# Performance work log

Hardware: AMD Instinct MI355X
Metric: run time of the kernel (lower is better)

The kernel has to match this reference:

```python
import jax, jax.numpy as jnp
import numpy as np

B = 32          # batch
NR = 1000       # n_reports
NP = 2000       # n_paths (candidate codes per lookup matrix)
NC = 3000       # n_codes (valid path / code entries)
NSNIP = 20000   # n_snippets
RV = 20000      # report word vocab
CV = 50000      # code word vocab
QL = 50         # report length (words)
S = 100         # num_snippet per code
L = 60          # len_snippet (words per snippet)
E = 300         # word embedding dim
DD = 100        # dim_dense
K = 5           # k_max_pool
NEG = 1.0e12


def setup_inputs() -> dict:
    key = jax.random.key(0)
    ks = jax.random.split(key, 16)
    f = jnp.float32
    sc = lambda n: 1.0 / float(np.sqrt(n))
    inp = {}
    inp["r_idx"] = jax.random.randint(ks[0], (B,), 0, NR)
    inp["c_idx"] = jax.random.randint(ks[1], (B,), 0, NP)
    # lookup tables stored as float (cast to int inside forward, as in torch)
    inp["matrix"] = jax.random.randint(ks[2], (NR, NP), 0, NC).astype(f)
    inp["report_table"] = jax.random.randint(ks[3], (NR, QL), 0, RV).astype(f)
    inp["report_word_emb"] = jax.random.normal(ks[4], (RV, E), dtype=f)
    inp["idf_table"] = jax.random.uniform(ks[5], (RV, 1), dtype=f, minval=0.5, maxval=6.0)
    inp["code_table"] = jax.random.randint(ks[6], (NC, S), 0, NSNIP).astype(f)
    inp["snippet_table"] = jax.random.randint(ks[7], (NSNIP, L), 0, CV).astype(f)
    inp["code_word_emb"] = jax.random.normal(ks[8], (CV, E), dtype=f)
    inp["snippet_len_table"] = jax.random.randint(ks[9], (NSNIP, 1), 1, L + 1).astype(f)
    inp["code_len_table"] = jax.random.randint(ks[10], (NP, 1), 1, S + 1).astype(f)
    # trainable relevance MLP + k-max fusion
    inp["W1"] = jax.random.uniform(ks[11], (E, DD), dtype=f, minval=-sc(E), maxval=sc(E))
    inp["b1"] = jnp.zeros((DD,), f)
    inp["W2"] = jax.random.uniform(ks[12], (DD, DD // 2), dtype=f, minval=-sc(DD), maxval=sc(DD))
    inp["b2"] = jnp.zeros((DD // 2,), f)
    inp["W3"] = jax.random.uniform(ks[13], (DD // 2, 1), dtype=f, minval=-sc(DD // 2), maxval=sc(DD // 2))
    inp["b3"] = jnp.zeros((1,), f)
    inp["Wk"] = jax.random.uniform(ks[14], (K, 1), dtype=f, minval=-sc(K), maxval=sc(K))
    inp["bk"] = jnp.zeros((1,), f)
    return inp


def _l2norm(x, axis):
    n = jnp.linalg.norm(x, ord=2, axis=axis, keepdims=True)
    y = x / n
    return jnp.where(jnp.isnan(y), 0.0, y)  # torch: NaN-fix after div


def reference(r_idx, c_idx, matrix, report_table, report_word_emb, idf_table,
              code_table, snippet_table, code_word_emb, snippet_len_table,
              code_len_table, W1, b1, W2, b2, W3, b3, Wk, bk):
    trans_c = matrix[r_idx, c_idx].astype(jnp.int32)            # (b,)
    r_vec = report_table[r_idx].astype(jnp.int32)               # (b,q)
    r_emb = report_word_emb[r_vec]                              # (b,q,e)
    c_snip = code_table[trans_c].astype(jnp.int32)              # (b,s)
    s_len = snippet_len_table[c_snip, 0].astype(jnp.int32)      # (b,s)
    c_words = snippet_table[c_snip].astype(jnp.int32)           # (b,s,l)
    c_emb = code_word_emb[c_words]                              # (b,s,l,e)
    s_mask = jnp.arange(L)[None, None, :] < s_len[:, :, None]   # (b,s,l)
    # masked dot attention: every report word attends within each snippet
    scores = jnp.einsum('bqe,bsle->bqsl', r_emb, c_emb)
    scores = scores - (~s_mask)[:, None, :, :].astype(scores.dtype) * NEG
    a = jax.nn.softmax(scores, axis=3)
    attn_v = jnp.einsum('bqsl,bsle->bqse', a, c_emb)            # (b,q,s,e)
    nc = _l2norm(attn_v, 3)                                     # (b,q,s,e)
    nr = _l2norm(r_emb, 2)                                      # (b,q,e)
    rc = nr[:, :, None, :] * nc                                 # (b,q,s,e)
    h = jnp.tanh(rc @ W1 + b1)
    h = jnp.tanh(h @ W2 + b2)
    rel = jnp.tanh(h @ W3 + b3)[..., 0]                         # (b,q,s)
    c_len = code_len_table[c_idx, 0].astype(jnp.int32)          # (b,)
    c_mask = (jnp.arange(S)[None, :] < c_len[:, None]).astype(rel.dtype)
    rel = rel * c_mask[:, None, :]
    topk = jax.lax.top_k(rel, K)[0]                             # (b,q,k)
    r_c = (topk @ Wk + bk)[..., 0]                              # (b,q)
    r_idf = idf_table[r_vec, 0]                                 # (b,q)
    r_idf = jnp.where(r_idf == 0.0, -NEG, r_idf)
    r_idf = jax.nn.softmax(r_idf, axis=1)
    return jnp.sum(r_c * r_idf, axis=1)                         # (b,)
```

## Files before the change

### kernel.cpp

```cpp
#include <hip/hip_runtime.h>
#include <math.h>

typedef __attribute__((ext_vector_type(8))) _Float16 half8;
typedef __attribute__((ext_vector_type(4))) _Float16 half4v;
typedef __attribute__((ext_vector_type(4))) float f32x4;

constexpr int cB = 32, cNP = 2000, cS = 100, cL = 60, cE = 300;
constexpr int cQ = 50, cDD = 100, cDH = 50;
constexpr float cNEG = 1.0e12f;

constexpr size_t OFF_REL  = 0;
constexpr size_t OFF_RG   = 160000;
constexpr size_t OFF_RNRM = 640000;
constexpr size_t OFF_IDFW = 641600;
constexpr size_t OFF_W1TH = 643200;
constexpr size_t OFF_W1TL = 660224;
constexpr size_t OFF_W2TH = 677248;
constexpr size_t OFF_W2TL = 681344;

constexpr int LDS_CL    = 0;
constexpr int LDS_AL    = 72000;
constexpr int LDS_AVF   = 84000;
constexpr int LDS_G_HI  = 0;
constexpr int LDS_G_LO  = 40960;
constexpr int LDS_H1    = 84000;
constexpr int LDS_H2    = 116768;
constexpr int LDS_SCL   = 144000;
constexpr int LDS_WORDS = 144256;
constexpr int LDS_TOTAL = 144512;

__device__ __forceinline__ _Float16 h_hi(float f) { return (_Float16)f; }
__device__ __forceinline__ _Float16 h_lo(float f, _Float16 h) { return (_Float16)(f - (float)h); }
__device__ __forceinline__ int bswz(int cb, int row) {
    return (cb & ~127) | ((cb & 127) ^ ((row & 7) << 4));
}

__global__ void prep_weights(const float* __restrict__ W1, const float* __restrict__ W2,
                             _Float16* __restrict__ W1TH, _Float16* __restrict__ W1TL,
                             _Float16* __restrict__ W2TH, _Float16* __restrict__ W2TL)
{
    int tid = blockIdx.x * blockDim.x + threadIdx.x;
    int stride = gridDim.x * blockDim.x;
    for (int idx = tid; idx < 112 * 304; idx += stride) {
        int d = idx / 304, e = idx % 304;
        float w = (d < cDD && e < cE) ? W1[(size_t)e * cDD + d] : 0.f;
        _Float16 h = h_hi(w);
        W1TH[idx] = h; W1TL[idx] = h_lo(w, h);
    }
    for (int idx = tid; idx < 64 * 128; idx += stride) {
        int j = idx / 128, d = idx % 128;
        float w = (j < cDH && d < cDD) ? W2[(size_t)d * cDH + j] : 0.f;
        _Float16 h = h_hi(w);
        W2TH[idx] = h; W2TL[idx] = h_lo(w, h);
    }
}

__global__ __launch_bounds__(256) void prep_batch(
    const int* __restrict__ r_idx,
    const float* __restrict__ report_table,
    const float* __restrict__ report_word_emb,
    const float* __restrict__ idf_table,
    float* __restrict__ Rg, float* __restrict__ rnorm, float* __restrict__ idfw)
{
    int b = blockIdx.x, tid = threadIdx.x;
    __shared__ int rv[cQ];
    if (tid < cQ) rv[tid] = (int)report_table[(size_t)r_idx[b] * cQ + tid];
    __syncthreads();
    float* dst = Rg + (size_t)b * cQ * cE;
    for (int idx = tid; idx < cQ * 75; idx += 256) {
        int q = idx / 75, e4 = idx % 75;
        f32x4 v = *(const f32x4*)(report_word_emb + (size_t)rv[q] * cE + e4 * 4);
        *(f32x4*)(dst + (size_t)q * cE + e4 * 4) = v;
    }
    __syncthreads();
    if (tid < cQ) {
        const float* row = dst + (size_t)tid * cE;
        float ss = 0.f;
        for (int e = 0; e < cE; e += 4) {
            f32x4 v = *(const f32x4*)(row + e);
            ss += v[0]*v[0] + v[1]*v[1] + v[2]*v[2] + v[3]*v[3];
        }
        rnorm[b * cQ + tid] = sqrtf(ss);
    }
    if (tid < 64) {
        float x = -INFINITY;
        if (tid < cQ) {
            float w = idf_table[rv[tid]];
            x = (w == 0.0f) ? -cNEG : w;
        }
        float m = x;
        for (int o = 32; o; o >>= 1) m = fmaxf(m, __shfl_xor(m, o));
        float e = (tid < cQ) ? expf(x - m) : 0.f;
        float ssum = e;
        for (int o = 32; o; o >>= 1) ssum += __shfl_xor(ssum, o);
        if (tid < cQ) idfw[b * cQ + tid] = e / ssum;
    }
}

__global__ __launch_bounds__(512, 1) void kernelA(
    const int* __restrict__ r_idx, const int* __restrict__ c_idx,
    const float* __restrict__ matrix, const float* __restrict__ code_table,
    const float* __restrict__ snippet_table, const float* __restrict__ code_word_emb,
    const float* __restrict__ snippet_len_table,
    const float* __restrict__ Rg, const float* __restrict__ rnorm,
    const _Float16* __restrict__ W1TH, const _Float16* __restrict__ W1TL, const float* __restrict__ b1,
    const _Float16* __restrict__ W2TH, const _Float16* __restrict__ W2TL, const float* __restrict__ b2,
    const float* __restrict__ W3, const float* __restrict__ b3,
    float* __restrict__ rel_out)
{
    const int s = blockIdx.x, b = blockIdx.y;
    const int tid = threadIdx.x;
    const int lane = tid & 63, wid = tid >> 6;
    const int n = lane & 15, gl = lane >> 4;

    __shared__ __align__(16) unsigned char smem[LDS_TOTAL];
    int*   words = (int*)(smem + LDS_WORDS);
    float* sclp  = (float*)(smem + LDS_SCL);
    float* Cl    = (float*)(smem + LDS_CL);
    float* Alp   = (float*)(smem + LDS_AL);
    float* AVf   = (float*)(smem + LDS_AVF);

    const int rr = r_idx[b], cc = c_idx[b];
    const int code = (int)matrix[(size_t)rr * cNP + cc];
    const int snip = (int)code_table[(size_t)code * cS + s];
    const int slen = (int)snippet_len_table[snip];

    if (tid < cL) words[tid] = (int)snippet_table[(size_t)snip * cL + tid];
    if (tid < cQ) sclp[tid] = 0.f;
    __syncthreads();

    for (int idx = tid; idx < cL * 75; idx += 512) {
        int l = idx / 75, e4 = idx % 75;
        f32x4 v = *(const f32x4*)(code_word_emb + (size_t)words[l] * cE + e4 * 4);
        *(f32x4*)(Cl + l * 300 + e4 * 4) = v;
    }
    __syncthreads();

    {
        const int qt = tid >> 5, lt2 = tid & 31;
        float acc[4][2];
        #pragma unroll
        for (int i = 0; i < 4; i++)
            #pragma unroll
            for (int j = 0; j < 2; j++) acc[i][j] = 0.f;
        const float* rbase = Rg + (size_t)b * cQ * cE;
        const float* rrow[4];
        #pragma unroll
        for (int i = 0; i < 4; i++) {
            int q = qt + 16 * i;
            rrow[i] = rbase + (size_t)(q < cQ ? q : 0) * cE;
        }
        int lrow[2];
        #pragma unroll
        for (int j = 0; j < 2; j++) {
            int l = lt2 + 32 * j;
            lrow[j] = (l < cL) ? l : 0;
        }
        for (int e = 0; e < cE; e += 4) {
            f32x4 rv[4], cv[2];
            #pragma unroll
            for (int i = 0; i < 4; i++) rv[i] = *(const f32x4*)(rrow[i] + e);
            #pragma unroll
            for (int j = 0; j < 2; j++) cv[j] = *(const f32x4*)(Cl + lrow[j] * 300 + e);
            #pragma unroll
            for (int i = 0; i < 4; i++)
                #pragma unroll
                for (int j = 0; j < 2; j++)
                    acc[i][j] += rv[i][0] * cv[j][0] + rv[i][1] * cv[j][1] +
                                 rv[i][2] * cv[j][2] + rv[i][3] * cv[j][3];
        }
        #pragma unroll
        for (int i = 0; i < 4; i++) {
            int q = qt + 16 * i;
            if (q >= cQ) continue;
            #pragma unroll
            for (int j = 0; j < 2; j++) {
                int l = lt2 + 32 * j;
                if (l >= cL) continue;
                Alp[q * 60 + l] = acc[i][j] - ((l >= slen) ? cNEG : 0.f);
            }
        }
    }
    __syncthreads();

    {
        const int g2 = tid >> 2, k = tid & 3;
        if (g2 < cQ) {
            float v[15];
            float m = -INFINITY;
            #pragma unroll
            for (int t = 0; t < 15; t++) { v[t] = Alp[g2 * 60 + k + 4 * t]; m = fmaxf(m, v[t]); }
            m = fmaxf(m, __shfl_xor(m, 1));
            m = fmaxf(m, __shfl_xor(m, 2));
            float sum = 0.f;
            #pragma unroll
            for (int t = 0; t < 15; t++) { v[t] = expf(v[t] - m); sum += v[t]; }
            sum += __shfl_xor(sum, 1);
            sum += __shfl_xor(sum, 2);
            float inv = 1.0f / sum;
            #pragma unroll
            for (int t = 0; t < 15; t++) Alp[g2 * 60 + k + 4 * t] = v[t] * inv;
        }
    }
    __syncthreads();

    {
        const int qt3 = tid >> 5, et3 = tid & 31;
        const float* arow[4];
        int qv[4];
        #pragma unroll
        for (int i = 0; i < 4; i++) {
            int q = qt3 + 16 * i;
            qv[i] = q;
            arow[i] = Alp + (size_t)((q < cQ) ? q : 0) * 60;
        }
        int e4v[3], e4c[3];
        #pragma unroll
        for (int jj = 0; jj < 3; jj++) {
            e4v[jj] = et3 + 32 * jj;
            e4c[jj] = (e4v[jj] < 75) ? e4v[jj] : 0;
        }
        f32x4 acc4[4][3];
        #pragma unroll
        for (int i = 0; i < 4; i++)
            #pragma unroll
            for (int jj = 0; jj < 3; jj++) acc4[i][jj] = (f32x4){0.f, 0.f, 0.f, 0.f};
        for (int l = 0; l < cL; l++) {
            float av[4];
            #pragma unroll
            for (int i = 0; i < 4; i++) av[i] = arow[i][l];
            f32x4 cv[3];
            #pragma unroll
            for (int jj = 0; jj < 3; jj++) cv[jj] = *(const f32x4*)(Cl + l * 300 + e4c[jj] * 4);
            #pragma unroll
            for (int i = 0; i < 4; i++)
                #pragma unroll
                for (int jj = 0; jj < 3; jj++) {
                    acc4[i][jj][0] += av[i] * cv[jj][0];
                    acc4[i][jj][1] += av[i] * cv[jj][1];
                    acc4[i][jj][2] += av[i] * cv[jj][2];
                    acc4[i][jj][3] += av[i] * cv[jj][3];
                }
        }
        #pragma unroll
        for (int i = 0; i < 4; i++)
            #pragma unroll
            for (int jj = 0; jj < 3; jj++)
                if (e4v[jj] < 75 && qv[i] < cQ)
                    *(f32x4*)(AVf + qv[i] * 300 + e4v[jj] * 4) = acc4[i][jj];
    }
    __syncthreads();

    if (tid < 256) {
        const int qs = tid >> 4, es = tid & 15;
        #pragma unroll
        for (int jj = 0; jj < 5; jj++) {
            int e4 = es + 16 * jj;
            int e4cl = (e4 < 75) ? e4 : 0;
            #pragma unroll
            for (int i = 0; i < 4; i++) {
                int q = qs + 16 * i;
                int qcl = (q < cQ) ? q : 0;
                f32x4 v = *(const f32x4*)(AVf + qcl * 300 + e4cl * 4);
                bool valid = (e4 < 75) && (q < cQ);
                float dv = valid ? (v[0]*v[0] + v[1]*v[1] + v[2]*v[2] + v[3]*v[3]) : 0.f;
                dv += __shfl_xor(dv, 1);
                dv += __shfl_xor(dv, 2);
                dv += __shfl_xor(dv, 4);
                dv += __shfl_xor(dv, 8);
                if (es == 0 && q < cQ) sclp[q] += dv;
            }
        }
    }
    __syncthreads();

    if (tid < cQ) {
        float p = rnorm[b * cQ + tid] * sqrtf(sclp[tid]);
        sclp[tid] = (p > 0.f) ? (1.0f / p) : 0.f;
    }

    {
        const float* RgB = Rg + (size_t)b * cQ * cE;
        for (int idx = tid; idx < 64 * 80; idx += 512) {
            int q = idx / 80, e4 = idx % 80;
            half4v h4 = {0, 0, 0, 0}, l4 = {0, 0, 0, 0};
            if (q < cQ && e4 < 75) {
                f32x4 av4 = *(const f32x4*)(AVf + q * 300 + e4 * 4);
                f32x4 rv4 = *(const f32x4*)(RgB + (size_t)q * cE + e4 * 4);
                #pragma unroll
                for (int k = 0; k < 4; k++) {
                    float gf = av4[k] * rv4[k];
                    h4[k] = h_hi(gf);
                    l4[k] = h_lo(gf, h4[k]);
                }
            }
            int bo = q * 640 + bswz(8 * e4, q);
            *(half4v*)(smem + LDS_G_HI + bo) = h4;
            *(half4v*)(smem + LDS_G_LO + bo) = l4;
        }
    }
    __syncthreads();

    {
        const half8 z8 = {0,0,0,0,0,0,0,0};
        const int dt = wid;
        f32x4 accH[4];
        #pragma unroll
        for (int q2 = 0; q2 < 4; q2++) accH[q2] = (f32x4){0.f, 0.f, 0.f, 0.f};
        if (dt < 7) {
            #pragma unroll
            for (int ks = 0; ks < 10; ks++) {
                bool lv = (ks != 9) || (gl < 2);
                half8 gh[4], glo[4];
                #pragma unroll
                for (int q2 = 0; q2 < 4; q2++) {
                    gh[q2] = z8; glo[q2] = z8;
                    if (lv) {
                        int q = 16 * q2 + n;
                        int bo = q * 640 + bswz(64 * ks + 16 * gl, q);
                        gh[q2]  = *(const half8*)(smem + LDS_G_HI + bo);
                        glo[q2] = *(const half8*)(smem + LDS_G_LO + bo);
                    }
                }
                half8 wh = z8, wl = z8;
                if (lv) {
                    int d = 16 * dt + n;
                    wh = *(const half8*)(W1TH + (size_t)d * 304 + 32 * ks + 8 * gl);
                    wl = *(const half8*)(W1TL + (size_t)d * 304 + 32 * ks + 8 * gl);
                }
                #pragma unroll
                for (int q2 = 0; q2 < 4; q2++) {
                    accH[q2] = __builtin_amdgcn_mfma_f32_16x16x32_f16(gh[q2],  wh, accH[q2], 0, 0, 0);
                    accH[q2] = __builtin_amdgcn_mfma_f32_16x16x32_f16(gh[q2],  wl, accH[q2], 0, 0, 0);
                    accH[q2] = __builtin_amdgcn_mfma_f32_16x16x32_f16(glo[q2], wh, accH[q2], 0, 0, 0);
                }
            }
        }
        float* h1p = (float*)(smem + LDS_H1);
        if (dt < 7) {
            int d = 16 * dt + n;
            #pragma unroll
            for (int q2 = 0; q2 < 4; q2++)
                #pragma unroll
                for (int r = 0; r < 4; r++) {
                    int q = 16 * q2 + 4 * gl + r;
                    if (q < cQ) {
                        float v = (d < cDD) ? tanhf(accH[q2][r] * sclp[q] + b1[d]) : 0.f;
                        h1p[q * 128 + d] = v;
                    }
                }
        }
        for (int idx = tid; idx < cQ * 16; idx += 512) {
            int q = idx >> 4, d = 112 + (idx & 15);
            h1p[q * 128 + d] = 0.f;
        }
    }
    __syncthreads();

    {
        const float* h1p = (const float*)(smem + LDS_H1);
        const int jw = 16 * (wid & 3) + n;
        const int q2b = (wid >> 2) * 2;
        f32x4 accJ[2];
        #pragma unroll
        for (int t = 0; t < 2; t++) accJ[t] = (f32x4){0.f, 0.f, 0.f, 0.f};
        #pragma unroll
        for (int ks = 0; ks < 4; ks++) {
            half8 hh[2], hl[2];
            #pragma unroll
            for (int t = 0; t < 2; t++) {
                int q = 16 * (q2b + t) + n;
                const float* p = h1p + q * 128 + 32 * ks + 8 * gl;
                f32x4 fa = *(const f32x4*)p;
                f32x4 fb = *(const f32x4*)(p + 4);
                half8 h8, l8;
                #pragma unroll
                for (int jj = 0; jj < 8; jj++) {
                    float f = (jj < 4) ? fa[jj] : fb[jj - 4];
                    _Float16 h = h_hi(f);
                    h8[jj] = h;
                    l8[jj] = h_lo(f, h);
                }
                hh[t] = h8; hl[t] = l8;
            }
            half8 wh = *(const half8*)(W2TH + (size_t)jw * 128 + 32 * ks + 8 * gl);
            half8 wl = *(const half8*)(W2TL + (size_t)jw * 128 + 32 * ks + 8 * gl);
            #pragma unroll
            for (int t = 0; t < 2; t++) {
                accJ[t] = __builtin_amdgcn_mfma_f32_16x16x32_f16(hh[t], wh, accJ[t], 0, 0, 0);
                accJ[t] = __builtin_amdgcn_mfma_f32_16x16x32_f16(hh[t], wl, accJ[t], 0, 0, 0);
                accJ[t] = __builtin_amdgcn_mfma_f32_16x16x32_f16(hl[t], wh, accJ[t], 0, 0, 0);
            }
        }
        float* h2p = (float*)(smem + LDS_H2);
        #pragma unroll
        for (int t = 0; t < 2; t++)
            #pragma unroll
            for (int r = 0; r < 4; r++) {
                int q = 16 * (q2b + t) + 4 * gl + r;
                if (q < cQ && jw < cDH) h2p[q * 68 + jw] = tanhf(accJ[t][r] + b2[jw]);
            }
    }
    __syncthreads();

    if (tid < cQ) {
        const float* h2p = (const float*)(smem + LDS_H2);
        float a = b3[0];
        #pragma unroll 10
        for (int jj = 0; jj < cDH; jj++) a += h2p[tid * 68 + jj] * W3[jj];
        rel_out[((size_t)b * cQ + tid) * cS + s] = tanhf(a);
    }
}

__global__ __launch_bounds__(64) void kernelB(
    const float* __restrict__ rel_ws, const float* __restrict__ idfw,
    const int* __restrict__ c_idx, const float* __restrict__ code_len_table,
    const float* __restrict__ Wk, const float* __restrict__ bk,
    float* __restrict__ out)
{
    int b = blockIdx.x, q = threadIdx.x;
    float val = 0.f;
    if (q < cQ) {
        int clen = (int)code_len_table[c_idx[b]];
        const float* row = rel_ws + ((size_t)b * cQ + q) * cS;
        float t0 = -INFINITY, t1 = -INFINITY, t2 = -INFINITY, t3 = -INFINITY, t4 = -INFINITY;
        for (int s = 0; s < cS; s++) {
            float v = row[s] * ((s < clen) ? 1.f : 0.f);
            float m0 = fmaxf(t0, v), n0 = fminf(t0, v);
            float m1 = fmaxf(t1, n0), n1 = fminf(t1, n0);
            float m2 = fmaxf(t2, n1), n2 = fminf(t2, n1);
            float m3 = fmaxf(t3, n2), n3 = fminf(t3, n2);
            float m4 = fmaxf(t4, n3);
            t0 = m0; t1 = m1; t2 = m2; t3 = m3; t4 = m4;
        }
        float rc = t0 * Wk[0] + t1 * Wk[1] + t2 * Wk[2] + t3 * Wk[3] + t4 * Wk[4] + bk[0];
        val = rc * idfw[b * cQ + q];
    }
    for (int o = 32; o; o >>= 1) val += __shfl_down(val, o);
    if (q == 0) out[b] = val;
}

extern "C" void kernel_launch(void* const* d_in, const int* in_sizes, int n_in,
                              void* d_out, int out_size, void* d_ws, size_t ws_size,
                              hipStream_t stream)
{
    const int*   r_idx             = (const int*)d_in[0];
    const int*   c_idx             = (const int*)d_in[1];
    const float* matrix            = (const float*)d_in[2];
    const float* report_table      = (const float*)d_in[3];
    const float* report_word_emb   = (const float*)d_in[4];
    const float* idf_table         = (const float*)d_in[5];
    const float* code_table        = (const float*)d_in[6];
    const float* snippet_table     = (const float*)d_in[7];
    const float* code_word_emb     = (const float*)d_in[8];
    const float* snippet_len_table = (const float*)d_in[9];
    const float* code_len_table    = (const float*)d_in[10];
    const float* W1 = (const float*)d_in[11];
    const float* b1 = (const float*)d_in[12];
    const float* W2 = (const float*)d_in[13];
    const float* b2 = (const float*)d_in[14];
    const float* W3 = (const float*)d_in[15];
    const float* b3 = (const float*)d_in[16];
    const float* Wk = (const float*)d_in[17];
    const float* bk = (const float*)d_in[18];
    float* out = (float*)d_out;
    float* ws  = (float*)d_ws;

    float* rel_ws = ws + OFF_REL;
    float* Rg     = ws + OFF_RG;
    float* rnormp = ws + OFF_RNRM;
    float* idfwp  = ws + OFF_IDFW;
    _Float16* W1THp = (_Float16*)(ws + OFF_W1TH);
    _Float16* W1TLp = (_Float16*)(ws + OFF_W1TL);
    _Float16* W2THp = (_Float16*)(ws + OFF_W2TH);
    _Float16* W2TLp = (_Float16*)(ws + OFF_W2TL);

    prep_weights<<<64, 256, 0, stream>>>(W1, W2, W1THp, W1TLp, W2THp, W2TLp);
    prep_batch<<<cB, 256, 0, stream>>>(r_idx, report_table, report_word_emb, idf_table,
                                       Rg, rnormp, idfwp);
    kernelA<<<dim3(cS, cB), 512, 0, stream>>>(r_idx, c_idx, matrix, code_table,
                                              snippet_table, code_word_emb, snippet_len_table,
                                              Rg, rnormp,
                                              W1THp, W1TLp, b1, W2THp, W2TLp, b2, W3, b3, rel_ws);
    kernelB<<<cB, 64, 0, stream>>>(rel_ws, idfwp, c_idx, code_len_table, Wk, bk, out);
}
```

Measured before the change: 622.1 us.

## Double kernelA block to 1024 threads and stage report embeddings in LDS

Launches kernelA with 1024 threads per block instead of 512. Every stage's per-thread work is halved: fewer query rows per thread in the score and attention GEMMs, and fewer MFMA tiles per wave in the MLP layers. The report embedding rows are now copied into LDS, reusing the AVf region before it is written, so the score loop reads LDS instead of global memory. The aim is more waves in flight to hide latency. The trade-off is a tighter register budget under the new launch bounds, and a larger block can limit how many blocks fit on a CU.

New measurement: 558.0 us. -10.3%, faster.

```diff
diff --git a/kernel.cpp b/kernel.cpp
--- a/kernel.cpp
+++ b/kernel.cpp
@@ -97,7 +97,7 @@
     }
 }
 
-__global__ __launch_bounds__(512, 1) void kernelA(
+__global__ __launch_bounds__(1024, 4) void kernelA(
     const int* __restrict__ r_idx, const int* __restrict__ c_idx,
     const float* __restrict__ matrix, const float* __restrict__ code_table,
     const float* __restrict__ snippet_table, const float* __restrict__ code_word_emb,
@@ -119,6 +119,7 @@
     float* Cl    = (float*)(smem + LDS_CL);
     float* Alp   = (float*)(smem + LDS_AL);
     float* AVf   = (float*)(smem + LDS_AVF);
+    float* Rlds  = (float*)(smem + LDS_AVF);
 
     const int rr = r_idx[b], cc = c_idx[b];
     const int code = (int)matrix[(size_t)rr * cNP + cc];
@@ -127,9 +128,16 @@
 
     if (tid < cL) words[tid] = (int)snippet_table[(size_t)snip * cL + tid];
     if (tid < cQ) sclp[tid] = 0.f;
-    __syncthreads();
-
-    for (int idx = tid; idx < cL * 75; idx += 512) {
+    {
+        const float* RgB = Rg + (size_t)b * cQ * cE;
+        for (int idx = tid; idx < cQ * 75; idx += 1024) {
+            int q = idx / 75, e4 = idx % 75;
+            *(f32x4*)(Rlds + q * 300 + e4 * 4) = *(const f32x4*)(RgB + (size_t)q * cE + e4 * 4);
+        }
+    }
+    __syncthreads();
+
+    for (int idx = tid; idx < cL * 75; idx += 1024) {
         int l = idx / 75, e4 = idx % 75;
         f32x4 v = *(const f32x4*)(code_word_emb + (size_t)words[l] * cE + e4 * 4);
         *(f32x4*)(Cl + l * 300 + e4 * 4) = v;
@@ -138,17 +146,16 @@
 
     {
         const int qt = tid >> 5, lt2 = tid & 31;
-        float acc[4][2];
-        #pragma unroll
-        for (int i = 0; i < 4; i++)
+        float acc[2][2];
+        #pragma unroll
+        for (int i = 0; i < 2; i++)
             #pragma unroll
             for (int j = 0; j < 2; j++) acc[i][j] = 0.f;
-        const float* rbase = Rg + (size_t)b * cQ * cE;
-        const float* rrow[4];
-        #pragma unroll
-        for (int i = 0; i < 4; i++) {
-            int q = qt + 16 * i;
-            rrow[i] = rbase + (size_t)(q < cQ ? q : 0) * cE;
+        const float* rrow[2];
+        #pragma unroll
+        for (int i = 0; i < 2; i++) {
+            int q = qt + 32 * i;
+            rrow[i] = Rlds + (size_t)(q < cQ ? q : 0) * 300;
         }
         int lrow[2];
         #pragma unroll
@@ -157,21 +164,21 @@
             lrow[j] = (l < cL) ? l : 0;
         }
         for (int e = 0; e < cE; e += 4) {
-            f32x4 rv[4], cv[2];
-            #pragma unroll
-            for (int i = 0; i < 4; i++) rv[i] = *(const f32x4*)(rrow[i] + e);
+            f32x4 rv[2], cv[2];
+            #pragma unroll
+            for (int i = 0; i < 2; i++) rv[i] = *(const f32x4*)(rrow[i] + e);
             #pragma unroll
             for (int j = 0; j < 2; j++) cv[j] = *(const f32x4*)(Cl + lrow[j] * 300 + e);
             #pragma unroll
-            for (int i = 0; i < 4; i++)
+            for (int i = 0; i < 2; i++)
                 #pragma unroll
                 for (int j = 0; j < 2; j++)
                     acc[i][j] += rv[i][0] * cv[j][0] + rv[i][1] * cv[j][1] +
                                  rv[i][2] * cv[j][2] + rv[i][3] * cv[j][3];
         }
         #pragma unroll
-        for (int i = 0; i < 4; i++) {
-            int q = qt + 16 * i;
+        for (int i = 0; i < 2; i++) {
+            int q = qt + 32 * i;
             if (q >= cQ) continue;
             #pragma unroll
             for (int j = 0; j < 2; j++) {
@@ -206,11 +213,11 @@
 
     {
         const int qt3 = tid >> 5, et3 = tid & 31;
-        const float* arow[4];
-        int qv[4];
-        #pragma unroll
-        for (int i = 0; i < 4; i++) {
-            int q = qt3 + 16 * i;
+        const float* arow[2];
+        int qv[2];
+        #pragma unroll
+        for (int i = 0; i < 2; i++) {
+            int q = qt3 + 32 * i;
             qv[i] = q;
             arow[i] = Alp + (size_t)((q < cQ) ? q : 0) * 60;
         }
@@ -220,20 +227,20 @@
             e4v[jj] = et3 + 32 * jj;
             e4c[jj] = (e4v[jj] < 75) ? e4v[jj] : 0;
         }
-        f32x4 acc4[4][3];
-        #pragma unroll
-        for (int i = 0; i < 4; i++)
+        f32x4 acc4[2][3];
+        #pragma unroll
+        for (int i = 0; i < 2; i++)
             #pragma unroll
             for (int jj = 0; jj < 3; jj++) acc4[i][jj] = (f32x4){0.f, 0.f, 0.f, 0.f};
         for (int l = 0; l < cL; l++) {
-            float av[4];
-            #pragma unroll
-            for (int i = 0; i < 4; i++) av[i] = arow[i][l];
+            float av[2];
+            #pragma unroll
+            for (int i = 0; i < 2; i++) av[i] = arow[i][l];
             f32x4 cv[3];
             #pragma unroll
             for (int jj = 0; jj < 3; jj++) cv[jj] = *(const f32x4*)(Cl + l * 300 + e4c[jj] * 4);
             #pragma unroll
-            for (int i = 0; i < 4; i++)
+            for (int i = 0; i < 2; i++)
                 #pragma unroll
                 for (int jj = 0; jj < 3; jj++) {
                     acc4[i][jj][0] += av[i] * cv[jj][0];
@@ -243,7 +250,7 @@
                 }
         }
         #pragma unroll
-        for (int i = 0; i < 4; i++)
+        for (int i = 0; i < 2; i++)
             #pragma unroll
             for (int jj = 0; jj < 3; jj++)
                 if (e4v[jj] < 75 && qv[i] < cQ)
@@ -281,7 +288,7 @@
 
     {
         const float* RgB = Rg + (size_t)b * cQ * cE;
-        for (int idx = tid; idx < 64 * 80; idx += 512) {
+        for (int idx = tid; idx < 64 * 80; idx += 1024) {
             int q = idx / 80, e4 = idx % 80;
             half4v h4 = {0, 0, 0, 0}, l4 = {0, 0, 0, 0};
             if (q < cQ && e4 < 75) {
@@ -303,23 +310,24 @@
 
     {
         const half8 z8 = {0,0,0,0,0,0,0,0};
-        const int dt = wid;
-        f32x4 accH[4];
-        #pragma unroll
-        for (int q2 = 0; q2 < 4; q2++) accH[q2] = (f32x4){0.f, 0.f, 0.f, 0.f};
+        const int dt = wid & 7;
+        const int q2b = (wid >> 3) * 2;
+        f32x4 accH[2];
+        #pragma unroll
+        for (int t = 0; t < 2; t++) accH[t] = (f32x4){0.f, 0.f, 0.f, 0.f};
         if (dt < 7) {
             #pragma unroll
             for (int ks = 0; ks < 10; ks++) {
                 bool lv = (ks != 9) || (gl < 2);
-                half8 gh[4], glo[4];
-                #pragma unroll
-                for (int q2 = 0; q2 < 4; q2++) {
-                    gh[q2] = z8; glo[q2] = z8;
+                half8 gh[2], glo[2];
+                #pragma unroll
+                for (int t = 0; t < 2; t++) {
+                    gh[t] = z8; glo[t] = z8;
                     if (lv) {
-                        int q = 16 * q2 + n;
+                        int q = 16 * (q2b + t) + n;
                         int bo = q * 640 + bswz(64 * ks + 16 * gl, q);
-                        gh[q2]  = *(const half8*)(smem + LDS_G_HI + bo);
-                        glo[q2] = *(const half8*)(smem + LDS_G_LO + bo);
+                        gh[t]  = *(const half8*)(smem + LDS_G_HI + bo);
+                        glo[t] = *(const half8*)(smem + LDS_G_LO + bo);
                     }
                 }
                 half8 wh = z8, wl = z8;
@@ -329,10 +337,10 @@
                     wl = *(const half8*)(W1TL + (size_t)d * 304 + 32 * ks + 8 * gl);
                 }
                 #pragma unroll
-                for (int q2 = 0; q2 < 4; q2++) {
-                    accH[q2] = __builtin_amdgcn_mfma_f32_16x16x32_f16(gh[q2],  wh, accH[q2], 0, 0, 0);
-                    accH[q2] = __builtin_amdgcn_mfma_f32_16x16x32_f16(gh[q2],  wl, accH[q2], 0, 0, 0);
-                    accH[q2] = __builtin_amdgcn_mfma_f32_16x16x32_f16(glo[q2], wh, accH[q2], 0, 0, 0);
+                for (int t = 0; t < 2; t++) {
+                    accH[t] = __builtin_amdgcn_mfma_f32_16x16x32_f16(gh[t],  wh, accH[t], 0, 0, 0);
+                    accH[t] = __builtin_amdgcn_mfma_f32_16x16x32_f16(gh[t],  wl, accH[t], 0, 0, 0);
+                    accH[t] = __builtin_amdgcn_mfma_f32_16x16x32_f16(glo[t], wh, accH[t], 0, 0, 0);
                 }
             }
         }
@@ -340,17 +348,17 @@
         if (dt < 7) {
             int d = 16 * dt + n;
             #pragma unroll
-            for (int q2 = 0; q2 < 4; q2++)
+            for (int t = 0; t < 2; t++)
                 #pragma unroll
                 for (int r = 0; r < 4; r++) {
-                    int q = 16 * q2 + 4 * gl + r;
+                    int q = 16 * (q2b + t) + 4 * gl + r;
                     if (q < cQ) {
-                        float v = (d < cDD) ? tanhf(accH[q2][r] * sclp[q] + b1[d]) : 0.f;
+                        float v = (d < cDD) ? tanhf(accH[t][r] * sclp[q] + b1[d]) : 0.f;
                         h1p[q * 128 + d] = v;
                     }
                 }
         }
-        for (int idx = tid; idx < cQ * 16; idx += 512) {
+        for (int idx = tid; idx < cQ * 16; idx += 1024) {
             int q = idx >> 4, d = 112 + (idx & 15);
             h1p[q * 128 + d] = 0.f;
         }
@@ -360,46 +368,34 @@
     {
         const float* h1p = (const float*)(smem + LDS_H1);
         const int jw = 16 * (wid & 3) + n;
-        const int q2b = (wid >> 2) * 2;
-        f32x4 accJ[2];
-        #pragma unroll
-        for (int t = 0; t < 2; t++) accJ[t] = (f32x4){0.f, 0.f, 0.f, 0.f};
+        const int q2 = wid >> 2;
+        f32x4 accJ = (f32x4){0.f, 0.f, 0.f, 0.f};
         #pragma unroll
         for (int ks = 0; ks < 4; ks++) {
-            half8 hh[2], hl[2];
-            #pragma unroll
-            for (int t = 0; t < 2; t++) {
-                int q = 16 * (q2b + t) + n;
-                const float* p = h1p + q * 128 + 32 * ks + 8 * gl;
-                f32x4 fa = *(const f32x4*)p;
-                f32x4 fb = *(const f32x4*)(p + 4);
-                half8 h8, l8;
-                #pragma unroll
-                for (int jj = 0; jj < 8; jj++) {
-                    float f = (jj < 4) ? fa[jj] : fb[jj - 4];
-                    _Float16 h = h_hi(f);
-                    h8[jj] = h;
-                    l8[jj] = h_lo(f, h);
-                }
-                hh[t] = h8; hl[t] = l8;
+            int q = 16 * q2 + n;
+            const float* p = h1p + q * 128 + 32 * ks + 8 * gl;
+            f32x4 fa = *(const f32x4*)p;
+            f32x4 fb = *(const f32x4*)(p + 4);
+            half8 h8, l8;
+            #pragma unroll
+            for (int jj = 0; jj < 8; jj++) {
+                float f = (jj < 4) ? fa[jj] : fb[jj - 4];
+                _Float16 h = h_hi(f);
+                h8[jj] = h;
+                l8[jj] = h_lo(f, h);
             }
             half8 wh = *(const half8*)(W2TH + (size_t)jw * 128 + 32 * ks + 8 * gl);
             half8 wl = *(const half8*)(W2TL + (size_t)jw * 128 + 32 * ks + 8 * gl);
-            #pragma unroll
-            for (int t = 0; t < 2; t++) {
-                accJ[t] = __builtin_amdgcn_mfma_f32_16x16x32_f16(hh[t], wh, accJ[t], 0, 0, 0);
-                accJ[t] = __builtin_amdgcn_mfma_f32_16x16x32_f16(hh[t], wl, accJ[t], 0, 0, 0);
-                accJ[t] = __builtin_amdgcn_mfma_f32_16x16x32_f16(hl[t], wh, accJ[t], 0, 0, 0);
-            }
+            accJ = __builtin_amdgcn_mfma_f32_16x16x32_f16(h8, wh, accJ, 0, 0, 0);
+            accJ = __builtin_amdgcn_mfma_f32_16x16x32_f16(h8, wl, accJ, 0, 0, 0);
+            accJ = __builtin_amdgcn_mfma_f32_16x16x32_f16(l8, wh, accJ, 0, 0, 0);
         }
         float* h2p = (float*)(smem + LDS_H2);
         #pragma unroll
-        for (int t = 0; t < 2; t++)
-            #pragma unroll
-            for (int r = 0; r < 4; r++) {
-                int q = 16 * (q2b + t) + 4 * gl + r;
-                if (q < cQ && jw < cDH) h2p[q * 68 + jw] = tanhf(accJ[t][r] + b2[jw]);
-            }
+        for (int r = 0; r < 4; r++) {
+            int q = 16 * q2 + 4 * gl + r;
+            if (q < cQ && jw < cDH) h2p[q * 68 + jw] = tanhf(accJ[r] + b2[jw]);
+        }
     }
     __syncthreads();
 
@@ -478,9 +474,9 @@
     prep_weights<<<64, 256, 0, stream>>>(W1, W2, W1THp, W1TLp, W2THp, W2TLp);
     prep_batch<<<cB, 256, 0, stream>>>(r_idx, report_table, report_word_emb, idf_table,
                                        Rg, rnormp, idfwp);
-    kernelA<<<dim3(cS, cB), 512, 0, stream>>>(r_idx, c_idx, matrix, code_table,
-                                              snippet_table, code_word_emb, snippet_len_table,
-                                              Rg, rnormp,
-                                              W1THp, W1TLp, b1, W2THp, W2TLp, b2, W3, b3, rel_ws);
+    kernelA<<<dim3(cS, cB), 1024, 0, stream>>>(r_idx, c_idx, matrix, code_table,
+                                               snippet_table, code_word_emb, snippet_len_table,
+                                               Rg, rnormp,
+                                               W1THp, W1TLp, b1, W2THp, W2TLp, b2, W3, b3, rel_ws);
     kernelB<<<cB, 64, 0, stream>>>(rel_ws, idfwp, c_idx, code_len_table, Wk, bk, out);
 }
```
